# Optimization experiments

Hardware: AMD Instinct MI355X
Metric: run time of the kernel (lower is better)

## Reference

```python
import jax, jax.numpy as jnp
import numpy as np

IN_FEATURES = 212445
NODE_SIZES = [IN_FEATURES, 65536, 16384, 128]
N_CLASSES = 20
BATCH = 32


def setup_inputs() -> dict:
    key = jax.random.key(0)
    ks = jax.random.split(key, 16)
    inp = {
        "x": jax.random.normal(ks[0], (BATCH, IN_FEATURES), dtype=jnp.float32),
        "W0": jax.random.normal(ks[1], (32, 1), dtype=jnp.float32) * 0.1,
        "b0": jax.random.normal(ks[2], (32,), dtype=jnp.float32) * 0.1,
        "W1": jax.random.normal(ks[3], (64, 32), dtype=jnp.float32) * 0.1,
        "b1": jax.random.normal(ks[4], (64,), dtype=jnp.float32) * 0.1,
        "W2": jax.random.normal(ks[5], (128, 64), dtype=jnp.float32) * 0.1,
        "b2": jax.random.normal(ks[6], (128,), dtype=jnp.float32) * 0.1,
        "fc_w": jax.random.normal(ks[7], (N_CLASSES, 128 * 128), dtype=jnp.float32) * 0.01,
        "fc_b": jax.random.normal(ks[8], (N_CLASSES,), dtype=jnp.float32) * 0.01,
        # random-tree adjacency: each input node has one parent output node
        "parent0": jax.random.randint(ks[9], (NODE_SIZES[0],), 0, NODE_SIZES[1], dtype=jnp.int32),
        "parent1": jax.random.randint(ks[10], (NODE_SIZES[1],), 0, NODE_SIZES[2], dtype=jnp.int32),
        "parent2": jax.random.randint(ks[11], (NODE_SIZES[2],), 0, NODE_SIZES[3], dtype=jnp.int32),
    }
    return inp


def _fgl(z, parent, n_out, W, b):
    """FGL layer: tree-adjacency reduction over nodes + channel mix.
    z: [N, C_in, n_in] -> [N, C_out, n_out]
    """
    N, C, n_in = z.shape
    # segment-sum reduce input nodes into their parent output node
    zt = jnp.moveaxis(z, 2, 0).reshape(n_in, N * C)          # [n_in, N*C]
    s = jax.ops.segment_sum(zt, parent, num_segments=n_out)  # [n_out, N*C]
    s = jnp.moveaxis(s.reshape(n_out, N, C), 0, 2)           # [N, C_in, n_out]
    # channel mixing (weight-normed linear over channels, shared across nodes)
    return jnp.einsum("oc,ncj->noj", W, s) + b[None, :, None]


def reference(x, W0, b0, W1, b1, W2, b2, fc_w, fc_b, parent0, parent1, parent2):
    N = x.shape[0]
    z = x[:, None, :]                                   # [N, 1, in_features]
    z = _fgl(z, parent0, NODE_SIZES[1], W0, b0)         # [N, 32, 65536]
    z = _fgl(z, parent1, NODE_SIZES[2], W1, b1)         # [N, 64, 16384]
    z = _fgl(z, parent2, NODE_SIZES[3], W2, b2)         # [N, 128, 128]
    logits = z.reshape(N, -1) @ fc_w.T + fc_b           # [N, n_classes]
    return logits
```

## Files before the change

kernel.cpp:

```cpp
#include <hip/hip_runtime.h>

#define IN_FEATURES 212445
#define N1 65536
#define N2 16384
#define NCLS 20
#define BATCH 32


__global__ __launch_bounds__(256) void k_setup(
    const float* __restrict__ W0, const float* __restrict__ b0,
    const float* __restrict__ W1, const float* __restrict__ b1,
    const float* __restrict__ W2,
    const int* __restrict__ p1, const int* __restrict__ p2,
    int* __restrict__ c2i, int* __restrict__ cnt2i,
    float* __restrict__ u1, float* __restrict__ v1,
    float* __restrict__ u2, float* __restrict__ v2, float* __restrict__ w2)
{
    int t = threadIdx.x;
    if (blockIdx.x == 0) {
        __shared__ float su1[64], sv1[64];
        if (t < 64) {
            float a = 0.f, b = 0.f;
            for (int c = 0; c < 32; ++c) {
                float w = W1[t * 32 + c];
                a += w * W0[c];
                b += w * b0[c];
            }
            su1[t] = a; sv1[t] = b;
            u1[t] = a; v1[t] = b;
        }
        __syncthreads();
        if (t < 128) {
            float a = 0.f, b = 0.f, c = 0.f;
            for (int j = 0; j < 64; ++j) {
                float w = W2[t * 64 + j];
                a += w * su1[j];
                b += w * sv1[j];
                c += w * b1[j];
            }
            u2[t] = a; v2[t] = b; w2[t] = c;
        }
    } else {
        __shared__ int hA[128], hB[128];
        if (t < 128) { hA[t] = 0; hB[t] = 0; }
        __syncthreads();
        const int total = N1 + N2;
        const int stride = (gridDim.x - 1) * blockDim.x;
        for (int idx = (blockIdx.x - 1) * blockDim.x + t; idx < total; idx += stride) {
            if (idx < N1) {
                int m = p2[p1[idx]];
                atomicAdd(&hA[m], 1);
            } else {
                int m = p2[idx - N1];
                atomicAdd(&hB[m], 1);
            }
        }
        __syncthreads();
        if (t < 128)      atomicAdd(&c2i[t], hA[t]);
        else              atomicAdd(&cnt2i[t - 128], hB[t - 128]);
    }
}

__global__ __launch_bounds__(256) void k_t3(
    const float* __restrict__ x,
    const int* __restrict__ p0, const int* __restrict__ p1,
    const int* __restrict__ p2, float* __restrict__ t3)
{
    __shared__ float acc[8 * 128];
    int t = threadIdx.x;
    for (int s = t; s < 1024; s += 256) acc[s] = 0.f;
    __syncthreads();

    int g  = blockIdx.x & 3;
    int cb = blockIdx.x >> 2;
    int base_row = g * 8;

    for (int i = cb * 256 + t; i < IN_FEATURES; i += 128 * 256) {
        int m = p2[p1[p0[i]]];
        const float* xp = x + i;
        #pragma unroll
        for (int r = 0; r < 8; ++r) {
            float v = xp[(base_row + r) * IN_FEATURES];
            atomicAdd(&acc[r * 128 + m], v);
        }
    }
    __syncthreads();
    for (int s = t; s < 1024; s += 256) {
        int r = s >> 7, m = s & 127;
        atomicAdd(&t3[(base_row + r) * 128 + m], acc[s]);
    }
}

__global__ __launch_bounds__(128) void k_A(
    const float* __restrict__ fc_w, const float* __restrict__ fc_b,
    const float* __restrict__ b2,
    const float* __restrict__ u2, const float* __restrict__ v2,
    const float* __restrict__ w2,
    const int* __restrict__ c2i, const int* __restrict__ cnt2i,
    float* __restrict__ A, float* __restrict__ constv)
{
    __shared__ float su[128], sv[128], sw[128], sb[128];
    __shared__ float red[128];
    int m = threadIdx.x;
    su[m] = u2[m]; sv[m] = v2[m]; sw[m] = w2[m]; sb[m] = b2[m];
    __syncthreads();

    int cls = blockIdx.x;
    const float* fw = fc_w + cls * 16384 + m;
    float Sa = 0.f, Sv = 0.f, Sw = 0.f, Sb = 0.f;
    for (int o = 0; o < 128; ++o) {
        float w = fw[o * 128];
        Sa += w * su[o];
        Sv += w * sv[o];
        Sw += w * sw[o];
        Sb += w * sb[o];
    }
    A[cls * 128 + m] = Sa;
    red[m] = (float)c2i[m] * Sv + (float)cnt2i[m] * Sw + Sb;
    __syncthreads();
    for (int s = 64; s > 0; s >>= 1) {
        if (m < s) red[m] += red[m + s];
        __syncthreads();
    }
    if (m == 0) constv[cls] = red[0] + fc_b[cls];
}

__global__ __launch_bounds__(640) void k_logits(
    const float* __restrict__ t3, const float* __restrict__ A,
    const float* __restrict__ constv, float* __restrict__ out)
{
    int tid = threadIdx.x;
    if (tid < BATCH * NCLS) {
        int n = tid / NCLS, cls = tid % NCLS;
        const float* tr = t3 + n * 128;
        const float* ar = A + cls * 128;
        float s = constv[cls];
        for (int m = 0; m < 128; ++m) s += ar[m] * tr[m];
        out[n * NCLS + cls] = s;
    }
}

extern "C" void kernel_launch(void* const* d_in, const int* in_sizes, int n_in,
                              void* d_out, int out_size, void* d_ws, size_t ws_size,
                              hipStream_t stream)
{
    const float* x    = (const float*)d_in[0];
    const float* W0   = (const float*)d_in[1];
    const float* b0   = (const float*)d_in[2];
    const float* W1   = (const float*)d_in[3];
    const float* b1   = (const float*)d_in[4];
    const float* W2   = (const float*)d_in[5];
    const float* b2   = (const float*)d_in[6];
    const float* fc_w = (const float*)d_in[7];
    const float* fc_b = (const float*)d_in[8];
    const int*   p0   = (const int*)d_in[9];
    const int*   p1   = (const int*)d_in[10];
    const int*   p2   = (const int*)d_in[11];

    char* ws = (char*)d_ws;
    float* t3     = (float*)(ws + 0);
    int*   c2i    = (int*)(ws + 16384);
    int*   cnt2i  = (int*)(ws + 16896);
    float* u1     = (float*)(ws + 17408);
    float* v1     = (float*)(ws + 17664);
    float* u2     = (float*)(ws + 17920);
    float* v2     = (float*)(ws + 18432);
    float* w2     = (float*)(ws + 18944);
    float* A      = (float*)(ws + 19456);
    float* constv = (float*)(ws + 29696);

    hipMemsetAsync(ws, 0, 17408, stream);

    k_setup<<<9, 256, 0, stream>>>(W0, b0, W1, b1, W2, p1, p2,
                                   c2i, cnt2i, u1, v1, u2, v2, w2);
    k_t3<<<512, 256, 0, stream>>>(x, p0, p1, p2, t3);
    k_A<<<20, 128, 0, stream>>>(fc_w, fc_b, b2, u2, v2, w2, c2i, cnt2i, A, constv);
    k_logits<<<1, 640, 0, stream>>>(t3, A, constv, (float*)d_out);
}
```

Measured before the change: 162.5 us.

## Drop memset, fuse logits into final kernel, restructure t3 to all-batch blocks

```diff
diff --git a/kernel.cpp b/kernel.cpp
--- a/kernel.cpp
+++ b/kernel.cpp
@@ -5,6 +5,7 @@
 #define N2 16384
 #define NCLS 20
 #define BATCH 32
+#define HIST_BLOCKS 16
 
 
 __global__ __launch_bounds__(256) void k_setup(
@@ -12,52 +13,47 @@
     const float* __restrict__ W1, const float* __restrict__ b1,
     const float* __restrict__ W2,
     const int* __restrict__ p1, const int* __restrict__ p2,
-    int* __restrict__ c2i, int* __restrict__ cnt2i,
-    float* __restrict__ u1, float* __restrict__ v1,
+    float* __restrict__ t3, int* __restrict__ hist,
     float* __restrict__ u2, float* __restrict__ v2, float* __restrict__ w2)
 {
     int t = threadIdx.x;
-    if (blockIdx.x == 0) {
+    int b = blockIdx.x;
+    if (b == 0) {
         __shared__ float su1[64], sv1[64];
         if (t < 64) {
-            float a = 0.f, b = 0.f;
+            float a = 0.f, bb = 0.f;
             for (int c = 0; c < 32; ++c) {
                 float w = W1[t * 32 + c];
-                a += w * W0[c];
-                b += w * b0[c];
+                a  += w * W0[c];
+                bb += w * b0[c];
             }
-            su1[t] = a; sv1[t] = b;
-            u1[t] = a; v1[t] = b;
+            su1[t] = a; sv1[t] = bb;
         }
         __syncthreads();
         if (t < 128) {
-            float a = 0.f, b = 0.f, c = 0.f;
+            float a = 0.f, bb = 0.f, c = 0.f;
             for (int j = 0; j < 64; ++j) {
                 float w = W2[t * 64 + j];
-                a += w * su1[j];
-                b += w * sv1[j];
-                c += w * b1[j];
+                a  += w * su1[j];
+                bb += w * sv1[j];
+                c  += w * b1[j];
             }
-            u2[t] = a; v2[t] = b; w2[t] = c;
+            u2[t] = a; v2[t] = bb; w2[t] = c;
         }
+    } else if (b == 1) {
+        for (int s = t; s < BATCH * 128; s += 256) t3[s] = 0.f;
     } else {
         __shared__ int hA[128], hB[128];
         if (t < 128) { hA[t] = 0; hB[t] = 0; }
         __syncthreads();
         const int total = N1 + N2;
-        const int stride = (gridDim.x - 1) * blockDim.x;
-        for (int idx = (blockIdx.x - 1) * blockDim.x + t; idx < total; idx += stride) {
-            if (idx < N1) {
-                int m = p2[p1[idx]];
-                atomicAdd(&hA[m], 1);
-            } else {
-                int m = p2[idx - N1];
-                atomicAdd(&hB[m], 1);
-            }
+        const int stride = HIST_BLOCKS * 256;
+        for (int idx = (b - 2) * 256 + t; idx < total; idx += stride) {
+            if (idx < N1) atomicAdd(&hA[p2[p1[idx]]], 1);
+            else          atomicAdd(&hB[p2[idx - N1]], 1);
         }
         __syncthreads();
-        if (t < 128)      atomicAdd(&c2i[t], hA[t]);
-        else              atomicAdd(&cnt2i[t - 128], hB[t - 128]);
+        hist[(b - 2) * 256 + t] = (t < 128) ? hA[t] : hB[t - 128];
     }
 }
 
@@ -66,48 +62,55 @@
     const int* __restrict__ p0, const int* __restrict__ p1,
     const int* __restrict__ p2, float* __restrict__ t3)
 {
-    __shared__ float acc[8 * 128];
+    __shared__ float acc[BATCH * 128];
     int t = threadIdx.x;
-    for (int s = t; s < 1024; s += 256) acc[s] = 0.f;
+    for (int s = t; s < BATCH * 128; s += 256) acc[s] = 0.f;
     __syncthreads();
 
-    int g  = blockIdx.x & 3;
-    int cb = blockIdx.x >> 2;
-    int base_row = g * 8;
-
-    for (int i = cb * 256 + t; i < IN_FEATURES; i += 128 * 256) {
+    for (int i = blockIdx.x * 256 + t; i < IN_FEATURES; i += 256 * 256) {
         int m = p2[p1[p0[i]]];
         const float* xp = x + i;
         #pragma unroll
-        for (int r = 0; r < 8; ++r) {
-            float v = xp[(base_row + r) * IN_FEATURES];
-            atomicAdd(&acc[r * 128 + m], v);
+        for (int r = 0; r < BATCH; ++r) {
+            atomicAdd(&acc[r * 128 + m], xp[r * IN_FEATURES]);
         }
     }
     __syncthreads();
-    for (int s = t; s < 1024; s += 256) {
-        int r = s >> 7, m = s & 127;
-        atomicAdd(&t3[(base_row + r) * 128 + m], acc[s]);
-    }
+    for (int s = t; s < BATCH * 128; s += 256)
+        atomicAdd(&t3[s], acc[s]);
 }
 
-__global__ __launch_bounds__(128) void k_A(
+__global__ __launch_bounds__(128) void k_final(
     const float* __restrict__ fc_w, const float* __restrict__ fc_b,
     const float* __restrict__ b2,
     const float* __restrict__ u2, const float* __restrict__ v2,
     const float* __restrict__ w2,
-    const int* __restrict__ c2i, const int* __restrict__ cnt2i,
-    float* __restrict__ A, float* __restrict__ constv)
+    const int* __restrict__ hist, const float* __restrict__ t3,
+    float* __restrict__ out)
 {
     __shared__ float su[128], sv[128], sw[128], sb[128];
-    __shared__ float red[128];
+    __shared__ float sA[128], red[128];
+    __shared__ float st3[BATCH * 129];
+    __shared__ float sconst;
     int m = threadIdx.x;
+    int cls = blockIdx.x;
+
     su[m] = u2[m]; sv[m] = v2[m]; sw[m] = w2[m]; sb[m] = b2[m];
+    for (int s = m; s < BATCH * 128; s += 128) {
+        int r = s >> 7, mm = s & 127;
+        st3[r * 129 + mm] = t3[s];
+    }
+    int c2 = 0, cn2 = 0;
+    #pragma unroll
+    for (int h = 0; h < HIST_BLOCKS; ++h) {
+        c2  += hist[h * 256 + m];
+        cn2 += hist[h * 256 + 128 + m];
+    }
     __syncthreads();
 
-    int cls = blockIdx.x;
     const float* fw = fc_w + cls * 16384 + m;
     float Sa = 0.f, Sv = 0.f, Sw = 0.f, Sb = 0.f;
+    #pragma unroll 4
     for (int o = 0; o < 128; ++o) {
         float w = fw[o * 128];
         Sa += w * su[o];
@@ -115,29 +118,26 @@
         Sw += w * sw[o];
         Sb += w * sb[o];
     }
-    A[cls * 128 + m] = Sa;
-    red[m] = (float)c2i[m] * Sv + (float)cnt2i[m] * Sw + Sb;
+    sA[m] = Sa;
+    red[m] = (float)c2 * Sv + (float)cn2 * Sw + Sb;
     __syncthreads();
     for (int s = 64; s > 0; s >>= 1) {
         if (m < s) red[m] += red[m + s];
         __syncthreads();
     }
-    if (m == 0) constv[cls] = red[0] + fc_b[cls];
-}
+    if (m == 0) sconst = red[0] + fc_b[cls];
+    __syncthreads();
 
-__global__ __launch_bounds__(640) void k_logits(
-    const float* __restrict__ t3, const float* __restrict__ A,
-    const float* __restrict__ constv, float* __restrict__ out)
-{
-    int tid = threadIdx.x;
-    if (tid < BATCH * NCLS) {
-        int n = tid / NCLS, cls = tid % NCLS;
-        const float* tr = t3 + n * 128;
-        const float* ar = A + cls * 128;
-        float s = constv[cls];
-        for (int m = 0; m < 128; ++m) s += ar[m] * tr[m];
-        out[n * NCLS + cls] = s;
-    }
+    int n = m >> 2, q = m & 3;
+    const float* tr = st3 + n * 129 + q * 32;
+    const float* ar = sA + q * 32;
+    float s = 0.f;
+    #pragma unroll
+    for (int k = 0; k < 32; ++k) s += ar[k] * tr[k];
+    red[m] = s;
+    __syncthreads();
+    if (q == 0)
+        out[n * NCLS + cls] = sconst + red[m] + red[m + 1] + red[m + 2] + red[m + 3];
 }
 
 extern "C" void kernel_launch(void* const* d_in, const int* in_sizes, int n_in,
@@ -158,22 +158,15 @@
     const int*   p2   = (const int*)d_in[11];
 
     char* ws = (char*)d_ws;
-    float* t3     = (float*)(ws + 0);
-    int*   c2i    = (int*)(ws + 16384);
-    int*   cnt2i  = (int*)(ws + 16896);
-    float* u1     = (float*)(ws + 17408);
-    float* v1     = (float*)(ws + 17664);
-    float* u2     = (float*)(ws + 17920);
-    float* v2     = (float*)(ws + 18432);
-    float* w2     = (float*)(ws + 18944);
-    float* A      = (float*)(ws + 19456);
-    float* constv = (float*)(ws + 29696);
+    float* t3   = (float*)(ws + 0);
+    int*   hist = (int*)(ws + 16384);
+    float* u2   = (float*)(ws + 32768);
+    float* v2   = (float*)(ws + 33280);
+    float* w2   = (float*)(ws + 33792);
 
-    hipMemsetAsync(ws, 0, 17408, stream);
-
-    k_setup<<<9, 256, 0, stream>>>(W0, b0, W1, b1, W2, p1, p2,
-                                   c2i, cnt2i, u1, v1, u2, v2, w2);
-    k_t3<<<512, 256, 0, stream>>>(x, p0, p1, p2, t3);
-    k_A<<<20, 128, 0, stream>>>(fc_w, fc_b, b2, u2, v2, w2, c2i, cnt2i, A, constv);
-    k_logits<<<1, 640, 0, stream>>>(t3, A, constv, (float*)d_out);
+    k_setup<<<2 + HIST_BLOCKS, 256, 0, stream>>>(W0, b0, W1, b1, W2, p1, p2,
+                                                 t3, hist, u2, v2, w2);
+    k_t3<<<256, 256, 0, stream>>>(x, p0, p1, p2, t3);
+    k_final<<<NCLS, 128, 0, stream>>>(fc_w, fc_b, b2, u2, v2, w2, hist, t3,
+                                      (float*)d_out);
 }
```

New measurement: 154.9 us. -4.7%, faster.
